# Optimization experiments

Hardware: AMD Instinct MI355X
Metric: run time of the kernel (lower is better)

The kernel has to match this reference:

```python
import jax, jax.numpy as jnp
import numpy as np

RGB_MEAN = jnp.array([0.4488, 0.4371, 0.404], dtype=jnp.float32)
RGB_RANGE = 255.0
N_FEATS = 64
N_RESBLOCKS = 16
SUPER_OUT = 100 * 16  # full SuperConv2d out_channels
RES_SCALE = 1.0


def conv2d(x, w, b):
    # x: [N,C,H,W], w: [O,I,3,3], SAME padding (pad=1)
    y = jax.lax.conv_general_dilated(
        x, w, window_strides=(1, 1), padding='SAME',
        dimension_numbers=('NCHW', 'OIHW', 'NCHW'))
    return y + b[None, :, None, None]


def setup_inputs() -> dict:
    key = jax.random.key(0)
    ks = jax.random.split(key, 12)
    N, C, H, W = 8, 3, 128, 128
    nf, nrb = N_FEATS, N_RESBLOCKS
    sd = 0.05  # weight std to keep activations bounded over 16 resblocks
    inp = {
        'x': jax.random.normal(ks[0], (N, C, H, W), jnp.float32) * 50.0 + 127.0,
        'head_w': jax.random.normal(ks[1], (nf, C, 3, 3), jnp.float32) * sd,
        'head_b': jnp.zeros((nf,), jnp.float32),
        'rb_w1': jax.random.normal(ks[2], (nrb, nf, nf, 3, 3), jnp.float32) * sd,
        'rb_b1': jnp.zeros((nrb, nf), jnp.float32),
        'rb_w2': jax.random.normal(ks[3], (nrb, nf, nf, 3, 3), jnp.float32) * sd,
        'rb_b2': jnp.zeros((nrb, nf), jnp.float32),
        'body_w': jax.random.normal(ks[4], (nf, nf, 3, 3), jnp.float32) * sd,
        'body_b': jnp.zeros((nf,), jnp.float32),
        'super_w': jax.random.normal(ks[5], (SUPER_OUT, nf, 3, 3), jnp.float32) * sd,
        'super_b': jnp.zeros((SUPER_OUT,), jnp.float32),
        'out_w': jax.random.normal(ks[6], (3, 100, 3, 3), jnp.float32) * sd,
        'out_b': jnp.zeros((3,), jnp.float32),
        'scale': 2,
    }
    return inp


def reference(x, head_w, head_b, rb_w1, rb_b1, rb_w2, rb_b2,
              body_w, body_b, super_w, super_b, out_w, out_b, scale):
    s = int(scale)
    mean = (RGB_RANGE * RGB_MEAN)[None, :, None, None]
    x = x - mean  # sub_mean (std = 1)
    h = conv2d(x, head_w, head_b)  # head: [N,64,H,W]

    def resblock(carry, params):
        w1, b1, w2, b2 = params
        r = jax.nn.relu(conv2d(carry, w1, b1))
        r = conv2d(r, w2, b2)
        return carry + RES_SCALE * r, None

    res, _ = jax.lax.scan(resblock, h, (rb_w1, rb_b1, rb_w2, rb_b2))
    res = conv2d(res, body_w, body_b)
    res = res + h

    # SuperConv2d: dynamic out channels = scale^2 * 100 (slice of full weight)
    out_nc = s * s * 100
    t = conv2d(res, super_w[:out_nc], super_b[:out_nc])  # [N, 100*s^2, H, W]

    # pixel_shuffle: out[i,j,k] = in[i//s, j//s, k*s^2 + (i%s)*s + (j%s)]
    # == standard depth-to-space with channel group ordering (k, a, b)
    N, _, H, W = t.shape
    t = t.reshape(N, 100, s, s, H, W)          # [N,100,a,b,H,W]
    t = t.transpose(0, 1, 4, 2, 5, 3)          # [N,100,H,a,W,b]
    t = t.reshape(N, 100, H * s, W * s)

    y = conv2d(t, out_w, out_b)                # [N,3,H*s,W*s]
    y = y + mean  # add_mean
    return y
```

## Files before the change

kernel.cpp:

```cpp
#include <hip/hip_runtime.h>
#include <hip/hip_bf16.h>

#define HH 128
#define WW 128

typedef _Float16 half4_t __attribute__((ext_vector_type(4)));
typedef _Float16 half8 __attribute__((ext_vector_type(8)));
typedef float f32x4 __attribute__((ext_vector_type(4)));

__global__ __launch_bounds__(256)
void wxform_k(const float* __restrict__ rb_w1, const float* __restrict__ rb_w2,
              const float* __restrict__ body_w, const float* __restrict__ super_w,
              _Float16* __restrict__ Wt) {
    const int per64 = 64 * 64 * 9;
    const int n64   = 33 * per64;
    const int total = n64 + 448 * 64 * 9;
    for (int i = blockIdx.x * 256 + threadIdx.x; i < total; i += gridDim.x * 256) {
        if (i < n64) {
            int l  = i / per64;
            int r  = i - l * per64;
            int ic = r & 63, oc = (r >> 6) & 63, tap = r >> 12;
            const float* src = (l < 16) ? (rb_w1 + (size_t)l * per64)
                             : (l < 32) ? (rb_w2 + (size_t)(l - 16) * per64)
                                        : body_w;
            Wt[i] = (_Float16)src[(oc * 64 + ic) * 9 + tap];
        } else {
            int r   = i - n64;
            int ic  = r & 63;
            int oc  = (r >> 6) % 448;
            int tap = (r >> 6) / 448;
            float v = (oc < 400) ? super_w[((size_t)oc * 64 + ic) * 9 + tap] : 0.f;
            Wt[i] = (_Float16)v;
        }
    }
}

__global__ __launch_bounds__(256)
void head_k(const float* __restrict__ x, const float* __restrict__ w,
            const float* __restrict__ b, _Float16* __restrict__ out) {
    int n  = blockIdx.z;
    int gx = blockIdx.x * 16 + (threadIdx.x & 15);
    int gy = blockIdx.y * 16 + (threadIdx.x >> 4);
    float msub[3] = {255.0f * 0.4488f, 255.0f * 0.4371f, 255.0f * 0.4040f};
    float iv[27];
#pragma unroll
    for (int c = 0; c < 3; ++c)
#pragma unroll
        for (int dy = 0; dy < 3; ++dy)
#pragma unroll
            for (int dx = 0; dx < 3; ++dx) {
                int yy = gy + dy - 1, xx = gx + dx - 1;
                float v = 0.f;
                if ((unsigned)yy < HH && (unsigned)xx < WW)
                    v = x[(((size_t)n * 3 + c) * HH + yy) * WW + xx] - msub[c];
                iv[c * 9 + dy * 3 + dx] = v;
            }
    for (int ocg = 0; ocg < 16; ++ocg) {
        half4_t o;
#pragma unroll
        for (int q = 0; q < 4; ++q) {
            int oc  = ocg * 4 + q;
            float a = b[oc];
#pragma unroll
            for (int t = 0; t < 27; ++t) a = fmaf(iv[t], w[oc * 27 + t], a);
            o[q] = (_Float16)a;
        }
        *(half4_t*)&out[((((size_t)n * 16 + ocg) * HH + gy) * WW + gx) * 4] = o;
    }
}

__global__ __launch_bounds__(256, 2)
void frb_k(const _Float16* __restrict__ in, const _Float16* __restrict__ W1,
           const _Float16* __restrict__ W2, const float* __restrict__ b1,
           const float* __restrict__ b2, _Float16* __restrict__ out) {
    __shared__ __align__(16) _Float16 sBuf[15360 + 18432];
    _Float16* sIn  = sBuf;
    _Float16* sMid = sBuf;
    _Float16* sW   = sBuf + 15360;

    int tid = threadIdx.x;
    int n = blockIdx.z, bx = blockIdx.x, by = blockIdx.y;
    int wv = tid >> 6, lane = tid & 63;
    int lx = lane & 15, lg = lane >> 4;

    int c0 = -1 + (wv >> 1) * 5;
    int p0 = -1 + (wv & 1) * 2;
    int r0 = (wv & 1) * 4;
    int hh = wv >> 1;

    for (int i = tid; i < 1920; i += 256) {
        int icg = i / 240, pl = i - icg * 240;
        int py = pl / 20, px = pl - py * 20;
        int gy = by * 8 + py - 2, gx = bx * 16 + px - 2;
        half8 v = {0, 0, 0, 0, 0, 0, 0, 0};
        if ((unsigned)gy < (unsigned)HH && (unsigned)gx < (unsigned)WW) {
            size_t base = ((((size_t)n * 16 + icg * 2) * HH + gy) * WW + gx) * 4;
            half4_t a = *(const half4_t*)&in[base];
            half4_t c = *(const half4_t*)&in[base + (size_t)HH * WW * 4];
            v[0] = a[0]; v[1] = a[1]; v[2] = a[2]; v[3] = a[3];
            v[4] = c[0]; v[5] = c[1]; v[6] = c[2]; v[7] = c[3];
        }
        *(half8*)&sIn[pl * 64 + ((icg ^ (pl & 7)) << 3)] = v;
    }
#define STAGE_W(Wsrc, h)                                                      \
    for (int i = tid; i < 2304; i += 256) {                                   \
        int g = i & 3, oc = (i >> 2) & 63, tap = i >> 8;                      \
        half8 v = *(const half8*)&Wsrc[(size_t)(tap * 64 + oc) * 64 + (h) * 32 + g * 8]; \
        *(half8*)&sW[(tap * 64 + oc) * 32 + ((g ^ (oc & 3)) << 3)] = v;       \
    }
    STAGE_W(W1, 0)
    __syncthreads();

    f32x4 acc1[5][4];
#pragma unroll
    for (int r = 0; r < 5; ++r)
#pragma unroll
        for (int t = 0; t < 4; ++t) acc1[r][t] = (f32x4){0.f, 0.f, 0.f, 0.f};

#define CONV1_CHUNK(h)                                                        \
    {                                                                         \
        int icg = (h) * 4 + lg;                                               \
        _Pragma("unroll")                                                     \
        for (int dx = 0; dx < 3; ++dx) {                                      \
            half8 Bf[7];                                                      \
            _Pragma("unroll")                                                 \
            for (int d = 0; d < 7; ++d) {                                     \
                int pl = (c0 + d + 1) * 20 + (p0 + lx + dx + 1);              \
                Bf[d] = *(const half8*)&sIn[pl * 64 + ((icg ^ (pl & 7)) << 3)]; \
            }                                                                 \
            _Pragma("unroll")                                                 \
            for (int dy = 0; dy < 3; ++dy) {                                  \
                int tap = dy * 3 + dx;                                        \
                half8 Af[4];                                                  \
                _Pragma("unroll")                                             \
                for (int t = 0; t < 4; ++t)                                   \
                    Af[t] = *(const half8*)&sW[(tap * 64 + t * 16 + lx) * 32 + ((lg ^ (lx & 3)) << 3)]; \
                _Pragma("unroll")                                             \
                for (int r = 0; r < 5; ++r)                                   \
                    _Pragma("unroll")                                         \
                    for (int t = 0; t < 4; ++t)                               \
                        acc1[r][t] = __builtin_amdgcn_mfma_f32_16x16x32_f16(  \
                            Af[t], Bf[r + dy], acc1[r][t], 0, 0, 0);          \
            }                                                                 \
        }                                                                     \
    }

    CONV1_CHUNK(0)
    __syncthreads();
    STAGE_W(W1, 1)
    __syncthreads();
    CONV1_CHUNK(1)
    half4_t rs[4][2];
#pragma unroll
    for (int r = 0; r < 4; ++r)
#pragma unroll
        for (int t = 0; t < 2; ++t) {
            int oc0 = hh * 32 + t * 16 + lg * 4;
            int pl  = (r0 + r + 2) * 20 + lx + 2;
            rs[r][t] = *(const half4_t*)&sIn[pl * 64 + (((oc0 >> 3) ^ (pl & 7)) << 3) + (oc0 & 4)];
        }
    __syncthreads();

    {
        int gcol = bx * 16 + p0 + lx;
        bool colok = (unsigned)gcol < (unsigned)WW;
#pragma unroll
        for (int r = 0; r < 5; ++r) {
            int row  = c0 + r + 1;
            int grow = by * 8 + c0 + r;
            bool ok  = colok && ((unsigned)grow < (unsigned)HH);
#pragma unroll
            for (int t = 0; t < 4; ++t) {
                int oc0 = t * 16 + lg * 4;
                f32x4 bv = *(const f32x4*)&b1[oc0];
                int pl2 = row * 18 + (p0 + lx + 1);
                half4_t o;
#pragma unroll
                for (int q = 0; q < 4; ++q)
                    o[q] = ok ? (_Float16)fmaxf(acc1[r][t][q] + bv[q], 0.f)
                              : (_Float16)0.f;
                *(half4_t*)&sMid[pl2 * 64 + (((oc0 >> 3) ^ (pl2 & 7)) << 3) + (oc0 & 4)] = o;
            }
        }
    }
    STAGE_W(W2, 0)
    __syncthreads();

    f32x4 acc2[4][2];
#pragma unroll
    for (int r = 0; r < 4; ++r)
#pragma unroll
        for (int t = 0; t < 2; ++t) acc2[r][t] = (f32x4){0.f, 0.f, 0.f, 0.f};

#define CONV2_CHUNK(h)                                                        \
    {                                                                         \
        int icg = (h) * 4 + lg;                                               \
        _Pragma("unroll")                                                     \
        for (int dx = 0; dx < 3; ++dx) {                                      \
            half8 Bf[6];                                                      \
            _Pragma("unroll")                                                 \
            for (int d = 0; d < 6; ++d) {                                     \
                int pl = (r0 + d) * 18 + lx + dx;                             \
                Bf[d] = *(const half8*)&sMid[pl * 64 + ((icg ^ (pl & 7)) << 3)]; \
            }                                                                 \
            _Pragma("unroll")                                                 \
            for (int dy = 0; dy < 3; ++dy) {                                  \
                int tap = dy * 3 + dx;                                        \
                half8 Af[2];                                                  \
                _Pragma("unroll")                                             \
                for (int t = 0; t < 2; ++t) {                                 \
                    int oc = hh * 32 + t * 16 + lx;                           \
                    Af[t] = *(const half8*)&sW[(tap * 64 + oc) * 32 + ((lg ^ (lx & 3)) << 3)]; \
                }                                                             \
                _Pragma("unroll")                                             \
                for (int r = 0; r < 4; ++r)                                   \
                    _Pragma("unroll")                                         \
                    for (int t = 0; t < 2; ++t)                               \
                        acc2[r][t] = __builtin_amdgcn_mfma_f32_16x16x32_f16(  \
                            Af[t], Bf[r + dy], acc2[r][t], 0, 0, 0);          \
            }                                                                 \
        }                                                                     \
    }

    CONV2_CHUNK(0)
    __syncthreads();
    STAGE_W(W2, 1)
    __syncthreads();
    CONV2_CHUNK(1)
    {
        int gx0 = bx * 16 + lx;
#pragma unroll
        for (int r = 0; r < 4; ++r) {
            int y = by * 8 + r0 + r;
#pragma unroll
            for (int t = 0; t < 2; ++t) {
                int oc0 = hh * 32 + t * 16 + lg * 4;
                f32x4 bv = *(const f32x4*)&b2[oc0];
                size_t gi = ((((size_t)n * 16 + (oc0 >> 2)) * HH + y) * WW + gx0) * 4;
                half4_t o;
#pragma unroll
                for (int q = 0; q < 4; ++q)
                    o[q] = (_Float16)(acc2[r][t][q] + bv[q] + (float)rs[r][t][q]);
                *(half4_t*)&out[gi] = o;
            }
        }
    }
#undef STAGE_W
#undef CONV1_CHUNK
#undef CONV2_CHUNK
}

template<bool RES, bool NT>
__global__ __launch_bounds__(512, 2)
void mconv_k(const _Float16* __restrict__ in, const _Float16* __restrict__ Wt,
             const float* __restrict__ bias, const _Float16* __restrict__ resid,
             _Float16* __restrict__ out, int OCp, int OCr, int C4) {
    __shared__ __align__(16) _Float16 sIn[18 * 18 * 64];
    __shared__ __align__(16) _Float16 sW[9 * 32 * 64];

    int tid = threadIdx.x;
    int n = blockIdx.z, bx = blockIdx.x, by = blockIdx.y;

    for (int i = tid; i < 2592; i += 512) {
        int icg = i / 324, pl = i - icg * 324;
        int py = pl / 18, px = pl - py * 18;
        int gy = by * 16 + py - 1, gx = bx * 16 + px - 1;
        half8 v = {0, 0, 0, 0, 0, 0, 0, 0};
        if ((unsigned)gy < (unsigned)HH && (unsigned)gx < (unsigned)WW) {
            size_t base = ((((size_t)n * 16 + icg * 2) * HH + gy) * WW + gx) * 4;
            half4_t a = *(const half4_t*)&in[base];
            half4_t c = *(const half4_t*)&in[base + (size_t)HH * WW * 4];
            v[0] = a[0]; v[1] = a[1]; v[2] = a[2]; v[3] = a[3];
            v[4] = c[0]; v[5] = c[1]; v[6] = c[2]; v[7] = c[3];
        }
        *(half8*)&sIn[pl * 64 + ((icg ^ (pl & 7)) << 3)] = v;
    }
    __syncthreads();

    int wv = tid >> 6, lane = tid & 63;
    int lx = lane & 15, lg = lane >> 4;
    int r0 = wv * 2;
    int gx0 = bx * 16 + lx;

    for (int ocb = 0; ocb < OCp; ocb += 32) {
        __syncthreads();
        for (int i = tid; i < 2304; i += 512) {
            int tap = i >> 8, oc = (i >> 3) & 31, icg = i & 7;
            half8 v = *(const half8*)&Wt[((size_t)(tap * OCp + ocb + oc)) * 64 + icg * 8];
            *(half8*)&sW[(tap * 32 + oc) * 64 + ((icg ^ (oc & 7)) << 3)] = v;
        }
        __syncthreads();

        f32x4 acc[2][2];
#pragma unroll
        for (int r = 0; r < 2; ++r)
#pragma unroll
            for (int t = 0; t < 2; ++t) acc[r][t] = (f32x4){0.f, 0.f, 0.f, 0.f};

#pragma unroll
        for (int icstep = 0; icstep < 2; ++icstep) {
            int icoff = icstep * 32 + lg * 8;
            int icg   = icoff >> 3;
#pragma unroll
            for (int dx = 0; dx < 3; ++dx) {
                half8 Bf[4];
#pragma unroll
                for (int d = 0; d < 4; ++d) {
                    int pl = (r0 + d) * 18 + lx + dx;
                    Bf[d] = *(const half8*)&sIn[pl * 64 + ((icg ^ (pl & 7)) << 3)];
                }
#pragma unroll
                for (int dy = 0; dy < 3; ++dy) {
                    int tap = dy * 3 + dx;
                    half8 Af[2];
#pragma unroll
                    for (int t = 0; t < 2; ++t) {
                        int oc = t * 16 + lx;
                        Af[t] = *(const half8*)&sW[(tap * 32 + oc) * 64 + ((icg ^ (oc & 7)) << 3)];
                    }
#pragma unroll
                    for (int r = 0; r < 2; ++r)
#pragma unroll
                        for (int t = 0; t < 2; ++t)
                            acc[r][t] = __builtin_amdgcn_mfma_f32_16x16x32_f16(
                                Af[t], Bf[r + dy], acc[r][t], 0, 0, 0);
                }
            }
        }
#pragma unroll
        for (int r = 0; r < 2; ++r) {
            int y = by * 16 + r0 + r;
#pragma unroll
            for (int t = 0; t < 2; ++t) {
                int oc0 = ocb + t * 16 + lg * 4;
                if (oc0 >= OCr) continue;
                f32x4 bv = *(const f32x4*)&bias[oc0];
                size_t gi = ((((size_t)n * C4 + (oc0 >> 2)) * HH + y) * WW + gx0) * 4;
                float vv[4];
#pragma unroll
                for (int q = 0; q < 4; ++q) vv[q] = acc[r][t][q] + bv[q];
                if (RES) {
                    half4_t rg = *(const half4_t*)&resid[gi];
#pragma unroll
                    for (int q = 0; q < 4; ++q) vv[q] += (float)rg[q];
                }
                half4_t o;
#pragma unroll
                for (int q = 0; q < 4; ++q) o[q] = (_Float16)vv[q];
                if (NT) __builtin_nontemporal_store(o, (half4_t*)&out[gi]);
                else    *(half4_t*)&out[gi] = o;
            }
        }
    }
}

__global__ __launch_bounds__(256)
void out_k(const _Float16* __restrict__ S, const float* __restrict__ w,
           const float* __restrict__ b, float* __restrict__ out) {
    __shared__ __align__(8) _Float16 sG[10 * 18 * 18 * 4];
    int n = blockIdx.z;
    int tid = threadIdx.x;
    int ty = tid >> 4, tx = tid & 15;
    int a  = blockIdx.y * 16 + ty;
    int bc = blockIdx.x * 16 + tx;
    float acc[3][2][2];
#pragma unroll
    for (int c = 0; c < 3; ++c)
#pragma unroll
        for (int oy = 0; oy < 2; ++oy)
#pragma unroll
            for (int ox = 0; ox < 2; ++ox) acc[c][oy][ox] = 0.f;

    for (int ch = 0; ch < 10; ++ch) {
        __syncthreads();
        for (int i = tid; i < 3240; i += 256) {
            int ic = i / 324, pl = i - ic * 324;
            int py = pl / 18, px = pl - py * 18;
            int Y = blockIdx.y * 16 + py - 1, X = blockIdx.x * 16 + px - 1;
            half4_t v = {0, 0, 0, 0};
            if ((unsigned)Y < 128u && (unsigned)X < 128u)
                v = *(const half4_t*)&S[((((size_t)n * 100 + ch * 10 + ic) * 128 + Y) * 128 + X) * 4];
            *(half4_t*)&sG[(ic * 324 + pl) * 4] = v;
        }
        __syncthreads();
        for (int ic = 0; ic < 10; ++ic) {
            float g[3][3][4];
#pragma unroll
            for (int yi = 0; yi < 3; ++yi)
#pragma unroll
                for (int xi = 0; xi < 3; ++xi) {
                    half4_t hv = *(const half4_t*)&sG[((ic * 18 + ty + yi) * 18 + tx + xi) * 4];
#pragma unroll
                    for (int s = 0; s < 4; ++s) g[yi][xi][s] = (float)hv[s];
                }
            int icg = ch * 10 + ic;
#pragma unroll
            for (int oy = 0; oy < 2; ++oy)
#pragma unroll
                for (int ox = 0; ox < 2; ++ox)
#pragma unroll
                    for (int dy = 0; dy < 3; ++dy)
#pragma unroll
                        for (int dx = 0; dx < 3; ++dx) {
                            const int ey = oy + dy - 1, ex = ox + dx - 1;
                            const int yi = (ey >> 1) + 1, xi = (ex >> 1) + 1;
                            const int sub = (ey & 1) * 2 + (ex & 1);
                            float v = g[yi][xi][sub];
#pragma unroll
                            for (int c = 0; c < 3; ++c)
                                acc[c][oy][ox] = fmaf(v, w[(c * 100 + icg) * 9 + dy * 3 + dx],
                                                      acc[c][oy][ox]);
                        }
        }
    }
    const float madd[3] = {255.0f * 0.4488f, 255.0f * 0.4371f, 255.0f * 0.4040f};
#pragma unroll
    for (int c = 0; c < 3; ++c)
#pragma unroll
        for (int oy = 0; oy < 2; ++oy)
#pragma unroll
            for (int ox = 0; ox < 2; ++ox)
                out[(((size_t)n * 3 + c) * 256 + 2 * a + oy) * 256 + 2 * bc + ox] =
                    acc[c][oy][ox] + b[c] + madd[c];
}

extern "C" void kernel_launch(void* const* d_in, const int* in_sizes, int n_in,
                              void* d_out, int out_size, void* d_ws, size_t ws_size,
                              hipStream_t stream) {
    const float* x       = (const float*)d_in[0];
    const float* head_w  = (const float*)d_in[1];
    const float* head_b  = (const float*)d_in[2];
    const float* rb_w1   = (const float*)d_in[3];
    const float* rb_b1   = (const float*)d_in[4];
    const float* rb_w2   = (const float*)d_in[5];
    const float* rb_b2   = (const float*)d_in[6];
    const float* body_w  = (const float*)d_in[7];
    const float* body_b  = (const float*)d_in[8];
    const float* super_w = (const float*)d_in[9];
    const float* super_b = (const float*)d_in[10];
    const float* out_w   = (const float*)d_in[11];
    const float* out_b   = (const float*)d_in[12];
    float* out = (float*)d_out;

    const size_t ACT = (size_t)16777216;
    char* wsb = (char*)d_ws;
    _Float16* Tb = (_Float16*)wsb;
    _Float16* Hb = (_Float16*)(wsb + ACT);
    _Float16* Cb = (_Float16*)(wsb + 2 * ACT);
    _Float16* Sb = (_Float16*)(wsb + ACT);
    _Float16* Wt = (_Float16*)(wsb + ACT + 104857600);

    wxform_k<<<dim3(1440), 256, 0, stream>>>(rb_w1, rb_w2, body_w, super_w, Wt);

    head_k<<<dim3(8, 8, 8), 256, 0, stream>>>(x, head_w, head_b, Hb);

    const _Float16* Wt_bod = Wt + (size_t)32 * 36864;
    const _Float16* Wt_sup = Wt + (size_t)33 * 36864;

    const _Float16* cur = Hb;
    for (int i = 0; i < 16; ++i) {
        _Float16* dst = (i & 1) ? Cb : Tb;
        frb_k<<<dim3(8, 16, 8), 256, 0, stream>>>(
            cur, Wt + (size_t)i * 36864, Wt + (size_t)(16 + i) * 36864,
            rb_b1 + i * 64, rb_b2 + i * 64, dst);
        cur = dst;
    }
    mconv_k<true, false><<<dim3(8, 8, 8), 512, 0, stream>>>(
        Cb, Wt_bod, body_b, Hb, Tb, 64, 64, 16);
    mconv_k<false, true><<<dim3(8, 8, 8), 512, 0, stream>>>(
        Tb, Wt_sup, super_b, nullptr, Sb, 448, 400, 100);
    out_k<<<dim3(8, 8, 8), 256, 0, stream>>>(Sb, out_w, out_b, out);
}
```

Baseline: 1.007 ms.

## Fuse resblock chain into cooperative persistent kernel, prefetch weights, fp16 dot2 output conv

The 16 resblock launches become one cooperative persistent kernel with 512 blocks, each processing two tiles per layer and meeting at a grid sync between layers. Weight staging into LDS is now software-prefetched into registers while the previous chunk's MFMA work runs. The final output conv switches to fp16 pair-packed weights and input, using fdot2, with weights pre-converted in the transform kernel. These aim to cut launch gaps, weight-load stalls and FP32 FMA count, at the cost of more register pressure, grid-sync overhead and reduced accumulation precision.

```diff
diff --git a/kernel.cpp b/kernel.cpp
--- a/kernel.cpp
+++ b/kernel.cpp
@@ -1,9 +1,13 @@
 #include <hip/hip_runtime.h>
 #include <hip/hip_bf16.h>
+#include <hip/hip_cooperative_groups.h>
+
+namespace cg = cooperative_groups;
 
 #define HH 128
 #define WW 128
 
+typedef _Float16 half2_t __attribute__((ext_vector_type(2)));
 typedef _Float16 half4_t __attribute__((ext_vector_type(4)));
 typedef _Float16 half8 __attribute__((ext_vector_type(8)));
 typedef float f32x4 __attribute__((ext_vector_type(4)));
@@ -11,10 +15,12 @@
 __global__ __launch_bounds__(256)
 void wxform_k(const float* __restrict__ rb_w1, const float* __restrict__ rb_w2,
               const float* __restrict__ body_w, const float* __restrict__ super_w,
-              _Float16* __restrict__ Wt) {
+              const float* __restrict__ out_w,
+              _Float16* __restrict__ Wt, _Float16* __restrict__ Wo) {
     const int per64 = 64 * 64 * 9;
     const int n64   = 33 * per64;
-    const int total = n64 + 448 * 64 * 9;
+    const int nW    = n64 + 448 * 64 * 9;
+    const int total = nW + 1350;
     for (int i = blockIdx.x * 256 + threadIdx.x; i < total; i += gridDim.x * 256) {
         if (i < n64) {
             int l  = i / per64;
@@ -24,13 +30,19 @@
                              : (l < 32) ? (rb_w2 + (size_t)(l - 16) * per64)
                                         : body_w;
             Wt[i] = (_Float16)src[(oc * 64 + ic) * 9 + tap];
-        } else {
+        } else if (i < nW) {
             int r   = i - n64;
             int ic  = r & 63;
             int oc  = (r >> 6) % 448;
             int tap = (r >> 6) / 448;
             float v = (oc < 400) ? super_w[((size_t)oc * 64 + ic) * 9 + tap] : 0.f;
             Wt[i] = (_Float16)v;
+        } else {
+            int j = i - nW;
+            int c = j / 450, r = j - c * 450;
+            int p = r / 9, tap = r - p * 9;
+            Wo[j * 2]     = (_Float16)out_w[(c * 100 + 2 * p) * 9 + tap];
+            Wo[j * 2 + 1] = (_Float16)out_w[(c * 100 + 2 * p + 1) * 9 + tap];
         }
     }
 }
@@ -69,25 +81,41 @@
     }
 }
 
-__global__ __launch_bounds__(256, 2)
-void frb_k(const _Float16* __restrict__ in, const _Float16* __restrict__ W1,
-           const _Float16* __restrict__ W2, const float* __restrict__ b1,
-           const float* __restrict__ b2, _Float16* __restrict__ out) {
-    __shared__ __align__(16) _Float16 sBuf[15360 + 18432];
+__device__ __forceinline__ void frb_tile(
+    const _Float16* __restrict__ in, const _Float16* __restrict__ W1,
+    const _Float16* __restrict__ W2, const float* __restrict__ b1,
+    const float* __restrict__ b2, _Float16* __restrict__ out,
+    _Float16* sBuf, int tile) {
     _Float16* sIn  = sBuf;
     _Float16* sMid = sBuf;
     _Float16* sW   = sBuf + 15360;
 
     int tid = threadIdx.x;
-    int n = blockIdx.z, bx = blockIdx.x, by = blockIdx.y;
+    int bx = tile & 7, by = (tile >> 3) & 15, n = tile >> 7;
     int wv = tid >> 6, lane = tid & 63;
     int lx = lane & 15, lg = lane >> 4;
-
     int c0 = -1 + (wv >> 1) * 5;
     int p0 = -1 + (wv & 1) * 2;
     int r0 = (wv & 1) * 4;
     int hh = wv >> 1;
 
+    half8 pf[9];
+#define PF_W(Wsrc, h)                                                         \
+    _Pragma("unroll")                                                         \
+    for (int j = 0; j < 9; ++j) {                                             \
+        int i = tid + 256 * j;                                                \
+        int g = i & 3, oc = (i >> 2) & 63, tap = i >> 8;                      \
+        pf[j] = *(const half8*)&Wsrc[(size_t)(tap * 64 + oc) * 64 + (h) * 32 + g * 8]; \
+    }
+#define WR_W()                                                                \
+    _Pragma("unroll")                                                         \
+    for (int j = 0; j < 9; ++j) {                                             \
+        int i = tid + 256 * j;                                                \
+        int g = i & 3, oc = (i >> 2) & 63, tap = i >> 8;                      \
+        *(half8*)&sW[(tap * 64 + oc) * 32 + ((g ^ (oc & 3)) << 3)] = pf[j];   \
+    }
+
+    PF_W(W1, 0)
     for (int i = tid; i < 1920; i += 256) {
         int icg = i / 240, pl = i - icg * 240;
         int py = pl / 20, px = pl - py * 20;
@@ -102,13 +130,7 @@
         }
         *(half8*)&sIn[pl * 64 + ((icg ^ (pl & 7)) << 3)] = v;
     }
-#define STAGE_W(Wsrc, h)                                                      \
-    for (int i = tid; i < 2304; i += 256) {                                   \
-        int g = i & 3, oc = (i >> 2) & 63, tap = i >> 8;                      \
-        half8 v = *(const half8*)&Wsrc[(size_t)(tap * 64 + oc) * 64 + (h) * 32 + g * 8]; \
-        *(half8*)&sW[(tap * 64 + oc) * 32 + ((g ^ (oc & 3)) << 3)] = v;       \
-    }
-    STAGE_W(W1, 0)
+    WR_W()
     __syncthreads();
 
     f32x4 acc1[5][4];
@@ -117,16 +139,15 @@
 #pragma unroll
         for (int t = 0; t < 4; ++t) acc1[r][t] = (f32x4){0.f, 0.f, 0.f, 0.f};
 
-#define CONV1_CHUNK(h)                                                        \
+#define CONV1_CHUNK()                                                         \
     {                                                                         \
-        int icg = (h) * 4 + lg;                                               \
         _Pragma("unroll")                                                     \
         for (int dx = 0; dx < 3; ++dx) {                                      \
             half8 Bf[7];                                                      \
             _Pragma("unroll")                                                 \
             for (int d = 0; d < 7; ++d) {                                     \
                 int pl = (c0 + d + 1) * 20 + (p0 + lx + dx + 1);              \
-                Bf[d] = *(const half8*)&sIn[pl * 64 + ((icg ^ (pl & 7)) << 3)]; \
+                Bf[d] = *(const half8*)&sIn[pl * 64 + (((ch4 + lg) ^ (pl & 7)) << 3)]; \
             }                                                                 \
             _Pragma("unroll")                                                 \
             for (int dy = 0; dy < 3; ++dy) {                                  \
@@ -145,11 +166,13 @@
         }                                                                     \
     }
 
-    CONV1_CHUNK(0)
-    __syncthreads();
-    STAGE_W(W1, 1)
-    __syncthreads();
-    CONV1_CHUNK(1)
+    PF_W(W1, 1)
+    { const int ch4 = 0; CONV1_CHUNK() }
+    __syncthreads();
+    WR_W()
+    __syncthreads();
+    PF_W(W2, 0)
+    { const int ch4 = 4; CONV1_CHUNK() }
     half4_t rs[4][2];
 #pragma unroll
     for (int r = 0; r < 4; ++r)
@@ -183,7 +206,7 @@
             }
         }
     }
-    STAGE_W(W2, 0)
+    WR_W()
     __syncthreads();
 
     f32x4 acc2[4][2];
@@ -192,16 +215,15 @@
 #pragma unroll
         for (int t = 0; t < 2; ++t) acc2[r][t] = (f32x4){0.f, 0.f, 0.f, 0.f};
 
-#define CONV2_CHUNK(h)                                                        \
+#define CONV2_CHUNK()                                                         \
     {                                                                         \
-        int icg = (h) * 4 + lg;                                               \
         _Pragma("unroll")                                                     \
         for (int dx = 0; dx < 3; ++dx) {                                      \
             half8 Bf[6];                                                      \
             _Pragma("unroll")                                                 \
             for (int d = 0; d < 6; ++d) {                                     \
                 int pl = (r0 + d) * 18 + lx + dx;                             \
-                Bf[d] = *(const half8*)&sMid[pl * 64 + ((icg ^ (pl & 7)) << 3)]; \
+                Bf[d] = *(const half8*)&sMid[pl * 64 + (((ch4 + lg) ^ (pl & 7)) << 3)]; \
             }                                                                 \
             _Pragma("unroll")                                                 \
             for (int dy = 0; dy < 3; ++dy) {                                  \
@@ -222,11 +244,12 @@
         }                                                                     \
     }
 
-    CONV2_CHUNK(0)
-    __syncthreads();
-    STAGE_W(W2, 1)
-    __syncthreads();
-    CONV2_CHUNK(1)
+    PF_W(W2, 1)
+    { const int ch4 = 0; CONV2_CHUNK() }
+    __syncthreads();
+    WR_W()
+    __syncthreads();
+    { const int ch4 = 4; CONV2_CHUNK() }
     {
         int gx0 = bx * 16 + lx;
 #pragma unroll
@@ -245,9 +268,39 @@
             }
         }
     }
-#undef STAGE_W
+#undef PF_W
+#undef WR_W
 #undef CONV1_CHUNK
 #undef CONV2_CHUNK
+}
+
+__global__ __launch_bounds__(256, 2)
+void frbchain_k(const _Float16* __restrict__ Hb, _Float16* __restrict__ Tb,
+                _Float16* __restrict__ Cb, const _Float16* __restrict__ Wt,
+                const float* __restrict__ rb_b1, const float* __restrict__ rb_b2) {
+    __shared__ __align__(16) _Float16 sBuf[15360 + 18432];
+    cg::grid_group grid = cg::this_grid();
+    for (int l = 0; l < 16; ++l) {
+        const _Float16* src = (l == 0) ? Hb : ((l & 1) ? Tb : Cb);
+        _Float16* dst = (l & 1) ? Cb : Tb;
+        const _Float16* W1 = Wt + (size_t)l * 36864;
+        const _Float16* W2 = Wt + (size_t)(16 + l) * 36864;
+        frb_tile(src, W1, W2, rb_b1 + l * 64, rb_b2 + l * 64, dst, sBuf,
+                 (int)blockIdx.x);
+        __syncthreads();
+        frb_tile(src, W1, W2, rb_b1 + l * 64, rb_b2 + l * 64, dst, sBuf,
+                 (int)blockIdx.x + 512);
+        __threadfence();
+        grid.sync();
+    }
+}
+
+__global__ __launch_bounds__(256, 2)
+void frb1_k(const _Float16* __restrict__ in, const _Float16* __restrict__ W1,
+            const _Float16* __restrict__ W2, const float* __restrict__ b1,
+            const float* __restrict__ b2, _Float16* __restrict__ out) {
+    __shared__ __align__(16) _Float16 sBuf[15360 + 18432];
+    frb_tile(in, W1, W2, b1, b2, out, sBuf, (int)blockIdx.x);
 }
 
 template<bool RES, bool NT>
@@ -299,8 +352,7 @@
 
 #pragma unroll
         for (int icstep = 0; icstep < 2; ++icstep) {
-            int icoff = icstep * 32 + lg * 8;
-            int icg   = icoff >> 3;
+            int icg = icstep * 4 + lg;
 #pragma unroll
             for (int dx = 0; dx < 3; ++dx) {
                 half8 Bf[4];
@@ -355,9 +407,9 @@
 }
 
 __global__ __launch_bounds__(256)
-void out_k(const _Float16* __restrict__ S, const float* __restrict__ w,
+void out_k(const _Float16* __restrict__ S, const _Float16* __restrict__ Wo,
            const float* __restrict__ b, float* __restrict__ out) {
-    __shared__ __align__(8) _Float16 sG[10 * 18 * 18 * 4];
+    __shared__ __align__(16) _Float16 sG[5 * 324 * 8];
     int n = blockIdx.z;
     int tid = threadIdx.x;
     int ty = tid >> 4, tx = tid & 15;
@@ -373,27 +425,36 @@
 
     for (int ch = 0; ch < 10; ++ch) {
         __syncthreads();
-        for (int i = tid; i < 3240; i += 256) {
-            int ic = i / 324, pl = i - ic * 324;
+        for (int i = tid; i < 1620; i += 256) {
+            int p = i / 324, pl = i - p * 324;
             int py = pl / 18, px = pl - py * 18;
             int Y = blockIdx.y * 16 + py - 1, X = blockIdx.x * 16 + px - 1;
-            half4_t v = {0, 0, 0, 0};
-            if ((unsigned)Y < 128u && (unsigned)X < 128u)
-                v = *(const half4_t*)&S[((((size_t)n * 100 + ch * 10 + ic) * 128 + Y) * 128 + X) * 4];
-            *(half4_t*)&sG[(ic * 324 + pl) * 4] = v;
+            half4_t va = {0, 0, 0, 0}, vc = {0, 0, 0, 0};
+            if ((unsigned)Y < 128u && (unsigned)X < 128u) {
+                size_t base = ((((size_t)n * 100 + ch * 10 + p * 2) * 128 + Y) * 128 + X) * 4;
+                va = *(const half4_t*)&S[base];
+                vc = *(const half4_t*)&S[base + (size_t)128 * 128 * 4];
+            }
+            half8 v;
+            v[0] = va[0]; v[1] = vc[0]; v[2] = va[1]; v[3] = vc[1];
+            v[4] = va[2]; v[5] = vc[2]; v[6] = va[3]; v[7] = vc[3];
+            *(half8*)&sG[(p * 324 + pl) * 8] = v;
         }
         __syncthreads();
-        for (int ic = 0; ic < 10; ++ic) {
-            float g[3][3][4];
+#pragma unroll
+        for (int p = 0; p < 5; ++p) {
+            half2_t wv[3][9];
+#pragma unroll
+            for (int c = 0; c < 3; ++c)
+#pragma unroll
+                for (int t = 0; t < 9; ++t)
+                    wv[c][t] = *(const half2_t*)&Wo[((c * 50 + ch * 5 + p) * 9 + t) * 2];
+            half8 G[3][3];
 #pragma unroll
             for (int yi = 0; yi < 3; ++yi)
 #pragma unroll
-                for (int xi = 0; xi < 3; ++xi) {
-                    half4_t hv = *(const half4_t*)&sG[((ic * 18 + ty + yi) * 18 + tx + xi) * 4];
-#pragma unroll
-                    for (int s = 0; s < 4; ++s) g[yi][xi][s] = (float)hv[s];
-                }
-            int icg = ch * 10 + ic;
+                for (int xi = 0; xi < 3; ++xi)
+                    G[yi][xi] = *(const half8*)&sG[(p * 324 + (ty + yi) * 18 + tx + xi) * 8];
 #pragma unroll
             for (int oy = 0; oy < 2; ++oy)
 #pragma unroll
@@ -405,11 +466,12 @@
                             const int ey = oy + dy - 1, ex = ox + dx - 1;
                             const int yi = (ey >> 1) + 1, xi = (ex >> 1) + 1;
                             const int sub = (ey & 1) * 2 + (ex & 1);
-                            float v = g[yi][xi][sub];
+                            half8 g8 = G[yi][xi];
+                            half2_t gp = {g8[2 * sub], g8[2 * sub + 1]};
 #pragma unroll
                             for (int c = 0; c < 3; ++c)
-                                acc[c][oy][ox] = fmaf(v, w[(c * 100 + icg) * 9 + dy * 3 + dx],
-                                                      acc[c][oy][ox]);
+                                acc[c][oy][ox] = __builtin_amdgcn_fdot2(
+                                    gp, wv[c][dy * 3 + dx], acc[c][oy][ox], false);
                         }
         }
     }
@@ -449,25 +511,37 @@
     _Float16* Cb = (_Float16*)(wsb + 2 * ACT);
     _Float16* Sb = (_Float16*)(wsb + ACT);
     _Float16* Wt = (_Float16*)(wsb + ACT + 104857600);
-
-    wxform_k<<<dim3(1440), 256, 0, stream>>>(rb_w1, rb_w2, body_w, super_w, Wt);
+    _Float16* Wo = (_Float16*)(wsb + ACT + 104857600 + 2949120);
+
+    wxform_k<<<dim3(1440), 256, 0, stream>>>(rb_w1, rb_w2, body_w, super_w,
+                                             out_w, Wt, Wo);
 
     head_k<<<dim3(8, 8, 8), 256, 0, stream>>>(x, head_w, head_b, Hb);
 
     const _Float16* Wt_bod = Wt + (size_t)32 * 36864;
     const _Float16* Wt_sup = Wt + (size_t)33 * 36864;
 
-    const _Float16* cur = Hb;
-    for (int i = 0; i < 16; ++i) {
-        _Float16* dst = (i & 1) ? Cb : Tb;
-        frb_k<<<dim3(8, 16, 8), 256, 0, stream>>>(
-            cur, Wt + (size_t)i * 36864, Wt + (size_t)(16 + i) * 36864,
-            rb_b1 + i * 64, rb_b2 + i * 64, dst);
-        cur = dst;
+    {
+        const _Float16* aHb = Hb; _Float16* aTb = Tb; _Float16* aCb = Cb;
+        const _Float16* aWt = Wt; const float* ab1 = rb_b1; const float* ab2 = rb_b2;
+        void* args[] = {(void*)&aHb, (void*)&aTb, (void*)&aCb,
+                        (void*)&aWt, (void*)&ab1, (void*)&ab2};
+        hipError_t ce = hipLaunchCooperativeKernel((const void*)frbchain_k,
+                                                   dim3(512), dim3(256), args, 0, stream);
+        if (ce != hipSuccess) {
+            const _Float16* cur = Hb;
+            for (int i = 0; i < 16; ++i) {
+                _Float16* dst = (i & 1) ? Cb : Tb;
+                frb1_k<<<dim3(1024), 256, 0, stream>>>(
+                    cur, Wt + (size_t)i * 36864, Wt + (size_t)(16 + i) * 36864,
+                    rb_b1 + i * 64, rb_b2 + i * 64, dst);
+                cur = dst;
+            }
+        }
     }
     mconv_k<true, false><<<dim3(8, 8, 8), 512, 0, stream>>>(
         Cb, Wt_bod, body_b, Hb, Tb, 64, 64, 16);
     mconv_k<false, true><<<dim3(8, 8, 8), 512, 0, stream>>>(
         Tb, Wt_sup, super_b, nullptr, Sb, 448, 400, 100);
-    out_k<<<dim3(8, 8, 8), 256, 0, stream>>>(Sb, out_w, out_b, out);
-}
+    out_k<<<dim3(8, 8, 8), 256, 0, stream>>>(Sb, Wo, out_b, out);
+}
```

Result: slower. 3.175 ms (+215.2%).
